# Optimization experiments

Measured on AMD Instinct MI355X. Metric: run time of the kernel, lower is better.

Reference implementation:

```python
import jax, jax.numpy as jnp
import numpy as np
from jax import lax

T = 512
DELTA_T = 2.0 ** -10
MAX_RATE = 200.0
DECAY1, DECAY2, CONST, THRESH = 0.25, 0.25, 0.5, 0.3
B = 32


def _conv(x, w):
    # VALID 5x5 conv, stride 1, NCHW / OIHW
    return lax.conv_general_dilated(x, w, (1, 1), 'VALID',
                                    dimension_numbers=('NCHW', 'OIHW', 'NCHW'))


def _avgpool2(x):
    b, c, h, w = x.shape
    return x.reshape(b, c, h // 2, 2, w // 2, 2).mean(axis=(3, 5))


def _lif(drive, mem1, mem2, spike):
    # two-compartment LIF membrane update with soft reset via (1 - spike)
    mem1 = mem1 * DECAY1 * (1.0 - spike) + drive
    mem2 = mem2 * DECAY2 * (1.0 - spike) + CONST * mem1
    new_spike = (mem2 > THRESH).astype(drive.dtype)
    return mem1, mem2, new_spike


def setup_inputs() -> dict:
    key = jax.random.key(0)
    ks = jax.random.split(key, 6)
    image = jax.random.uniform(ks[0], (B, 1, 32, 32), dtype=jnp.float32)
    def kaiming(k, shape, fan_in):
        return jax.random.normal(k, shape, dtype=jnp.float32) / np.float32(np.sqrt(fan_in))
    w1 = kaiming(ks[1], (6, 1, 5, 5), 1 * 25)
    w2 = kaiming(ks[2], (16, 6, 5, 5), 6 * 25)
    w3 = kaiming(ks[3], (120, 16, 5, 5), 16 * 25)
    fw1 = kaiming(ks[4], (84, 120), 120)
    fw2 = kaiming(ks[5], (10, 84), 84)
    return {'image': image, 'w1': w1, 'w2': w2, 'w3': w3, 'fw1': fw1, 'fw2': fw2}


def reference(image, w1, w2, w3, fw1, fw2):
    dt = image.dtype
    z = lambda *s: (jnp.zeros(s, dt), jnp.zeros(s, dt), jnp.zeros(s, dt))
    state0 = (z(B, 6, 28, 28), z(B, 6, 14, 14), z(B, 16, 10, 10),
              z(B, 16, 5, 5), z(B, 120, 1, 1), z(B, 84), z(B, 10),
              jnp.zeros((B, 10), dt))
    keys = jax.random.split(jax.random.key(1), T)

    def step(state, k):
        s1, s2, s3, s4, s5, s6, s7, acc = state
        x = (image * MAX_RATE * DELTA_T > jax.random.uniform(k, image.shape, dtype=dt)).astype(dt)
        s1 = _lif(_conv(x, w1), *s1)
        s2 = _lif(_avgpool2(s1[2]), *s2)
        s3 = _lif(_conv(s2[2], w2), *s3)
        s4 = _lif(_avgpool2(s3[2]), *s4)
        s5 = _lif(_conv(s4[2], w3), *s5)
        s6 = _lif(s5[2].reshape(B, -1) @ fw1.T, *s6)
        s7 = _lif(s6[2] @ fw2.T, *s7)
        acc = acc + s7[2]
        return (s1, s2, s3, s4, s5, s6, s7, acc), None

    final, _ = lax.scan(step, state0, keys)
    return final[-1] / T
```

## Files before the change

### kernel.cpp

```cpp
#include <hip/hip_runtime.h>
#include <cstdint>

#define TSTEPS 512

typedef __attribute__((ext_vector_type(2))) float f32x2;

__device__ __forceinline__ void tfr(uint32_t& x0, uint32_t& x1, int r) {
    x0 += x1;
    x1 = (x1 << r) | (x1 >> (32 - r));
    x1 ^= x0;
}

__device__ __forceinline__ void threefry2x32(uint32_t k0, uint32_t k1,
                                             uint32_t c0, uint32_t c1,
                                             uint32_t& o0, uint32_t& o1) {
    uint32_t k2 = k0 ^ k1 ^ 0x1BD11BDAu;
    uint32_t x0 = c0 + k0, x1 = c1 + k1;
    tfr(x0, x1, 13); tfr(x0, x1, 15); tfr(x0, x1, 26); tfr(x0, x1, 6);
    x0 += k1; x1 += k2 + 1u;
    tfr(x0, x1, 17); tfr(x0, x1, 29); tfr(x0, x1, 16); tfr(x0, x1, 24);
    x0 += k2; x1 += k0 + 2u;
    tfr(x0, x1, 13); tfr(x0, x1, 15); tfr(x0, x1, 26); tfr(x0, x1, 6);
    x0 += k0; x1 += k1 + 3u;
    tfr(x0, x1, 17); tfr(x0, x1, 29); tfr(x0, x1, 16); tfr(x0, x1, 24);
    x0 += k1; x1 += k2 + 4u;
    tfr(x0, x1, 13); tfr(x0, x1, 15); tfr(x0, x1, 26); tfr(x0, x1, 6);
    o0 = x0 + k2; o1 = x1 + k0 + 5u;
}

__global__ void k_keys(uint2* __restrict__ keys) {
    int t = threadIdx.x;
    uint32_t o0, o1;
    threefry2x32(0u, 1u, 0u, (uint32_t)t, o0, o1);
    keys[t] = make_uint2(o0, o1);
}

__global__ __launch_bounds__(256) void k_encode(const float* __restrict__ img,
                                                const uint2* __restrict__ keys,
                                                uint32_t* __restrict__ sxm) {
    int gid = blockIdx.x * 256 + threadIdx.x;
    int t = gid >> 15;
    int n = gid & 32767;
    uint2 k = keys[t];
    uint32_t o0, o1;
    threefry2x32(k.x, k.y, 0u, (uint32_t)n, o0, o1);
    float u = __uint_as_float((o0 >> 9) | 0x3f800000u) - 1.0f;
    float p = (img[n] * 200.0f) * 0.0009765625f;
    unsigned long long bal = __ballot(p > u);
    if ((threadIdx.x & 63) == 0) {
        int word = n >> 5;
        sxm[t * 1024 + word]     = (uint32_t)bal;
        sxm[t * 1024 + word + 1] = (uint32_t)(bal >> 32);
    }
}

__device__ __forceinline__ void lif(float drive, float& m1, float& m2, float& sp) {
    float r = 1.0f - sp;
    m1 = m1 * 0.25f * r + drive;
    m2 = m2 * 0.25f * r + 0.5f * m1;
    sp = (m2 > 0.3f) ? 1.0f : 0.0f;
}

#define SMEM_DW 22606
#define SMEM_BYTES (SMEM_DW * 4)

__global__ __launch_bounds__(1024) void k_main(
        const float* __restrict__ w1g, const float* __restrict__ w2g,
        const float* __restrict__ w3g, const float* __restrict__ fw1g,
        const float* __restrict__ fw2g, const uint32_t* __restrict__ sxm,
        float* __restrict__ out) {
    extern __shared__ float smem[];
    const f32x2* tbl2v = (const f32x2*)smem;
    const f32x2* tbl1p = (const f32x2*)(smem + 15840);
    float*    fw2s  = smem + 16830;
    float*    s3f   = smem + 17670;
    float*    s4f   = smem + 20870;
    float*    s5f   = smem + 21670;
    float*    s6f   = smem + 21910;
    uint32_t* s1m   = (uint32_t*)(smem + 22078);
    uint32_t* s2m   = (uint32_t*)(smem + 22414);

    const int tid  = threadIdx.x;
    const int lane = tid & 63;
    const int b    = blockIdx.x;

    for (int e = tid; e < 990; e += 1024) {
        int pr = e / 330, r = e % 330;
        int ky = r / 66, r2 = r % 66;
        int m = r2 >> 1, half = r2 & 1;
        int c = pr * 2 + half;
        float v = 0.0f;
        #pragma unroll
        for (int kx = 0; kx < 5; ++kx)
            if ((m >> kx) & 1) v += w1g[c * 25 + ky * 5 + kx];
        smem[15840 + e] = v;
    }
    for (int e = tid; e < 7680; e += 1024) {
        int cg = e / 960, r = e % 960, ci = r / 160, r2 = r % 160;
        int ky = r2 >> 5, m = r2 & 31;
        float v0 = 0.0f, v1 = 0.0f;
        #pragma unroll
        for (int kx = 0; kx < 5; ++kx)
            if ((m >> kx) & 1) {
                v0 += w2g[((cg * 2) * 6 + ci) * 25 + ky * 5 + kx];
                v1 += w2g[((cg * 2 + 1) * 6 + ci) * 25 + ky * 5 + kx];
            }
        smem[2 * (((cg * 6 + ci) * 5 + ky) * 33 + m)]     = v0;
        smem[2 * (((cg * 6 + ci) * 5 + ky) * 33 + m) + 1] = v1;
    }
    for (int e = tid; e < 840; e += 1024) fw2s[e] = fw2g[e];
    for (int e = tid; e < 4936; e += 1024) smem[17670 + e] = 0.0f;

    float fw1r[15];
    if (tid < 672) {
        int o = tid >> 3, j = tid & 7;
        #pragma unroll
        for (int i = 0; i < 15; ++i) fw1r[i] = fw1g[o * 120 + j * 15 + i];
    }

    float m1a[6] = {}, m2a[6] = {}, spa[6] = {};
    float m1b0 = 0, m2b0 = 0, spb0 = 0, m1b1 = 0, m2b1 = 0, spb1 = 0;
    float m1c0 = 0, m2c0 = 0, spc0 = 0, m1c1 = 0, m2c1 = 0, spc1 = 0;
    float m1d = 0, m2d = 0, spd = 0;
    float m1e = 0, m2e = 0, spe = 0;
    float m1f = 0, m2f = 0, spf = 0;
    float m1g = 0, m2g = 0, spg = 0, accf = 0.0f;

    uint32_t sx_cur = 0u, sx_nxt = 0u;
    if (tid < 896) {
        int half = lane >> 5, row = lane & 31;
        sx_cur = sxm[half * 1024 + b * 32 + row];
        sx_nxt = sxm[(half + 2) * 1024 + b * 32 + row];
    }

    __syncthreads();

    #pragma unroll 1
    for (int tau = 0; tau < TSTEPS / 2 + 6; ++tau) {
        const int p = tau & 1, q = p ^ 1;

        if (tid < 896) {
            const int y = tid >> 5, x = tid & 31;
            const bool valid = (x < 28);
            #pragma unroll
            for (int u = 0; u < 2; ++u) {
                uint32_t* s1w = s1m + p * 336 + u * 168;
                f32x2 d01 = {0.0f, 0.0f}, d23 = {0.0f, 0.0f}, d45 = {0.0f, 0.0f};
                #pragma unroll
                for (int ky = 0; ky < 5; ++ky) {
                    uint32_t row = (uint32_t)__shfl((int)sx_cur, u * 32 + y + ky, 64);
                    uint32_t mm = (row >> x) & 31u;
                    d01 += tbl1p[(0 * 5 + ky) * 33 + mm];
                    d23 += tbl1p[(1 * 5 + ky) * 33 + mm];
                    d45 += tbl1p[(2 * 5 + ky) * 33 + mm];
                }
                lif(d01[0], m1a[0], m2a[0], spa[0]);
                lif(d01[1], m1a[1], m2a[1], spa[1]);
                lif(d23[0], m1a[2], m2a[2], spa[2]);
                lif(d23[1], m1a[3], m2a[3], spa[3]);
                lif(d45[0], m1a[4], m2a[4], spa[4]);
                lif(d45[1], m1a[5], m2a[5], spa[5]);
                #pragma unroll
                for (int c = 0; c < 6; ++c) {
                    unsigned long long bal = __ballot(valid && (spa[c] > 0.0f));
                    if (lane == 0)       s1w[c * 28 + (tid >> 6) * 2]     = (uint32_t)bal;
                    else if (lane == 32) s1w[c * 28 + (tid >> 6) * 2 + 1] = (uint32_t)(bal >> 32);
                }
            }
            sx_cur = sx_nxt;
            int tt = 2 * tau + 4 + (lane >> 5);
            if (tt > TSTEPS - 1) tt = TSTEPS - 1;
            sx_nxt = sxm[tt * 1024 + b * 32 + (lane & 31)];
        }

        #pragma unroll
        for (int u = 0; u < 2; ++u) {
            const uint32_t* s1r = s1m + q * 336 + u * 168;
            uint32_t*       s2w = s2m + p * 192 + u * 96;
            {
                const int c = tid / 224, rem = tid % 224;
                const int yy = rem >> 4, xx = rem & 15;
                const bool valid = (xx < 14);
                uint32_t r0 = s1r[c * 28 + 2 * yy];
                uint32_t r1 = s1r[c * 28 + 2 * yy + 1];
                uint32_t sh = 2u * (uint32_t)xx;
                int cnt = (int)((r0 >> sh) & 1u) + (int)((r0 >> (sh + 1)) & 1u)
                        + (int)((r1 >> sh) & 1u) + (int)((r1 >> (sh + 1)) & 1u);
                lif(0.25f * (float)cnt, m1b0, m2b0, spb0);
                unsigned long long bal = __ballot(valid && (spb0 > 0.0f));
                if ((lane & 15) == 0)
                    s2w[tid >> 4] = (uint32_t)((bal >> (lane & 48)) & 0x3FFFull);
            }
            if (tid >= 704) {
                const int slot = tid + 320;
                const int c = slot / 224, rem = slot % 224;
                const int yy = rem >> 4, xx = rem & 15;
                const bool valid = (xx < 14);
                uint32_t r0 = s1r[c * 28 + 2 * yy];
                uint32_t r1 = s1r[c * 28 + 2 * yy + 1];
                uint32_t sh = 2u * (uint32_t)xx;
                int cnt = (int)((r0 >> sh) & 1u) + (int)((r0 >> (sh + 1)) & 1u)
                        + (int)((r1 >> sh) & 1u) + (int)((r1 >> (sh + 1)) & 1u);
                lif(0.25f * (float)cnt, m1b1, m2b1, spb1);
                unsigned long long bal = __ballot(valid && (spb1 > 0.0f));
                if ((lane & 15) == 0)
                    s2w[slot >> 4] = (uint32_t)((bal >> (lane & 48)) & 0x3FFFull);
            }
        }

        if (tid >= 224) {
            const int uu = tid - 224;
            const int px = uu >> 3, cg = uu & 7;
            const int yy = px / 10, xx = px % 10;
            #pragma unroll
            for (int u = 0; u < 2; ++u) {
                const uint32_t* s2r = s2m + q * 192 + u * 96;
                float*          s3w = s3f + p * 3200 + u * 1600;
                f32x2 d01 = {0.0f, 0.0f};
                #pragma unroll
                for (int ci = 0; ci < 6; ++ci) {
                    #pragma unroll
                    for (int ky = 0; ky < 5; ++ky) {
                        uint32_t mm = (s2r[ci * 14 + yy + ky] >> xx) & 31u;
                        d01 += tbl2v[((cg * 6 + ci) * 5 + ky) * 33 + mm];
                    }
                }
                lif(d01[0], m1c0, m2c0, spc0);
                lif(d01[1], m1c1, m2c1, spc1);
                s3w[(cg * 2) * 100 + px]     = spc0;
                s3w[(cg * 2 + 1) * 100 + px] = spc1;
            }
        }

        if (tid < 400) {
            const int c = tid / 25, rem = tid % 25;
            const int yy = rem / 5, xx = rem % 5;
            #pragma unroll
            for (int u = 0; u < 2; ++u) {
                const float* pp = s3f + q * 3200 + u * 1600 + c * 100 + yy * 20 + xx * 2;
                float sum = pp[0] + pp[1] + pp[10] + pp[11];
                lif(0.25f * sum, m1d, m2d, spd);
                (s4f + p * 800 + u * 400)[tid] = spd;
            }
        }

        if (tid < 960) {
            const int cc = tid >> 3, j = tid & 7;
            const float2* wp  = (const float2*)(w3g + cc * 400 + j * 50);
            const float2* sp0 = (const float2*)(s4f + q * 800 + 0 * 400 + j * 50);
            const float2* sp1 = (const float2*)(s4f + q * 800 + 1 * 400 + j * 50);
            float sum0 = 0.0f, sum1 = 0.0f;
            #pragma unroll
            for (int i = 0; i < 25; ++i) {
                float2 w = wp[i];
                float2 a = sp0[i];
                float2 c2 = sp1[i];
                sum0 = fmaf(w.y, a.y,  fmaf(w.x, a.x,  sum0));
                sum1 = fmaf(w.y, c2.y, fmaf(w.x, c2.x, sum1));
            }
            sum0 += __shfl_xor(sum0, 1, 64);
            sum0 += __shfl_xor(sum0, 2, 64);
            sum0 += __shfl_xor(sum0, 4, 64);
            sum1 += __shfl_xor(sum1, 1, 64);
            sum1 += __shfl_xor(sum1, 2, 64);
            sum1 += __shfl_xor(sum1, 4, 64);
            if (j == 0) {
                lif(sum0, m1e, m2e, spe); (s5f + p * 240 + 0 * 120)[cc] = spe;
                lif(sum1, m1e, m2e, spe); (s5f + p * 240 + 1 * 120)[cc] = spe;
            }
        }

        if (tid < 672) {
            const int j = tid & 7;
            #pragma unroll
            for (int u = 0; u < 2; ++u) {
                const float* s5r = s5f + q * 240 + u * 120;
                float sum = 0.0f;
                #pragma unroll
                for (int i = 0; i < 15; ++i) sum = fmaf(fw1r[i], s5r[j * 15 + i], sum);
                sum += __shfl_xor(sum, 1, 64);
                sum += __shfl_xor(sum, 2, 64);
                sum += __shfl_xor(sum, 4, 64);
                if (j == 0) { lif(sum, m1f, m2f, spf); (s6f + p * 168 + u * 84)[tid >> 3] = spf; }
            }
        }

        if (tid < 40) {
            const int o = tid >> 2, j = tid & 3;
            #pragma unroll
            for (int u = 0; u < 2; ++u) {
                const float* s6r = s6f + q * 168 + u * 84;
                float sum = 0.0f;
                #pragma unroll
                for (int i = 0; i < 21; ++i)
                    sum = fmaf(fw2s[o * 84 + j * 21 + i], s6r[j * 21 + i], sum);
                sum += __shfl_xor(sum, 1, 64);
                sum += __shfl_xor(sum, 2, 64);
                if (j == 0) { lif(sum, m1g, m2g, spg); accf += spg; }
            }
        }

        __syncthreads();
    }

    if (tid < 40 && (tid & 3) == 0)
        out[b * 10 + (tid >> 2)] = accf * (1.0f / 512.0f);
}

extern "C" void kernel_launch(void* const* d_in, const int* in_sizes, int n_in,
                              void* d_out, int out_size, void* d_ws, size_t ws_size,
                              hipStream_t stream) {
    const float* img = (const float*)d_in[0];
    const float* w1  = (const float*)d_in[1];
    const float* w2  = (const float*)d_in[2];
    const float* w3  = (const float*)d_in[3];
    const float* fw1 = (const float*)d_in[4];
    const float* fw2 = (const float*)d_in[5];
    float* out = (float*)d_out;

    uint2*    keys = (uint2*)d_ws;
    uint32_t* sxm  = (uint32_t*)((char*)d_ws + 4096);

    k_keys<<<1, 512, 0, stream>>>(keys);
    k_encode<<<(TSTEPS * 32768) / 256, 256, 0, stream>>>(img, keys, sxm);

    (void)hipFuncSetAttribute(reinterpret_cast<const void*>(k_main),
                              hipFuncAttributeMaxDynamicSharedMemorySize,
                              SMEM_BYTES);
    k_main<<<32, 1024, SMEM_BYTES, stream>>>(w1, w2, w3, fw1, fw2, sxm, out);
}
```

Baseline: 2.093 ms.

## Rotate per-wave stage order to stagger pipeline stages across waves

Wraps the seven per-timestep layer stages in a loop with a switch keyed on (wave id + k) mod 7, so each wavefront runs the stages in a different rotated order. The goal is to spread out contention for the same LDS tables, global weights and ALU work, so waves are not all hitting the same resource at once. The conv1 table goes back to a plain scalar float layout and conv2 now uses float2 loads with scalar accumulation. The change adds a runtime switch and loop overhead, and it may hurt instruction-cache behaviour and register allocation because the stage code can no longer be straight-lined.

```diff
diff --git a/kernel.cpp b/kernel.cpp
--- a/kernel.cpp
+++ b/kernel.cpp
@@ -2,8 +2,6 @@
 #include <cstdint>
 
 #define TSTEPS 512
-
-typedef __attribute__((ext_vector_type(2))) float f32x2;
 
 __device__ __forceinline__ void tfr(uint32_t& x0, uint32_t& x1, int r) {
     x0 += x1;
@@ -70,8 +68,8 @@
         const float* __restrict__ fw2g, const uint32_t* __restrict__ sxm,
         float* __restrict__ out) {
     extern __shared__ float smem[];
-    const f32x2* tbl2v = (const f32x2*)smem;
-    const f32x2* tbl1p = (const f32x2*)(smem + 15840);
+    float2*   tbl2v = (float2*)smem;
+    float*    tbl1  = smem + 15840;
     float*    fw2s  = smem + 16830;
     float*    s3f   = smem + 17670;
     float*    s4f   = smem + 20870;
@@ -82,18 +80,16 @@
 
     const int tid  = threadIdx.x;
     const int lane = tid & 63;
+    const int wid  = tid >> 6;
     const int b    = blockIdx.x;
 
-    for (int e = tid; e < 990; e += 1024) {
-        int pr = e / 330, r = e % 330;
-        int ky = r / 66, r2 = r % 66;
-        int m = r2 >> 1, half = r2 & 1;
-        int c = pr * 2 + half;
+    for (int e = tid; e < 960; e += 1024) {
+        int c = e / 160, r = e % 160, ky = r >> 5, m = r & 31;
         float v = 0.0f;
         #pragma unroll
         for (int kx = 0; kx < 5; ++kx)
             if ((m >> kx) & 1) v += w1g[c * 25 + ky * 5 + kx];
-        smem[15840 + e] = v;
+        tbl1[(c * 5 + ky) * 33 + m] = v;
     }
     for (int e = tid; e < 7680; e += 1024) {
         int cg = e / 960, r = e % 960, ci = r / 160, r2 = r % 160;
@@ -105,8 +101,7 @@
                 v0 += w2g[((cg * 2) * 6 + ci) * 25 + ky * 5 + kx];
                 v1 += w2g[((cg * 2 + 1) * 6 + ci) * 25 + ky * 5 + kx];
             }
-        smem[2 * (((cg * 6 + ci) * 5 + ky) * 33 + m)]     = v0;
-        smem[2 * (((cg * 6 + ci) * 5 + ky) * 33 + m) + 1] = v1;
+        tbl2v[((cg * 6 + ci) * 5 + ky) * 33 + m] = make_float2(v0, v1);
     }
     for (int e = tid; e < 840; e += 1024) fw2s[e] = fw2g[e];
     for (int e = tid; e < 4936; e += 1024) smem[17670 + e] = 0.0f;
@@ -139,164 +134,181 @@
     for (int tau = 0; tau < TSTEPS / 2 + 6; ++tau) {
         const int p = tau & 1, q = p ^ 1;
 
-        if (tid < 896) {
-            const int y = tid >> 5, x = tid & 31;
-            const bool valid = (x < 28);
+        #pragma unroll 1
+        for (int k = 0; k < 7; ++k) {
+            switch ((wid + k) % 7) {
+            case 0:
+            if (tid < 896) {
+                const int y = tid >> 5, x = tid & 31;
+                const bool valid = (x < 28);
+                #pragma unroll
+                for (int u = 0; u < 2; ++u) {
+                    uint32_t* s1w = s1m + p * 336 + u * 168;
+                    float d[6];
+                    #pragma unroll
+                    for (int c = 0; c < 6; ++c) d[c] = 0.0f;
+                    #pragma unroll
+                    for (int ky = 0; ky < 5; ++ky) {
+                        uint32_t row = (uint32_t)__shfl((int)sx_cur, u * 32 + y + ky, 64);
+                        uint32_t mm = (row >> x) & 31u;
+                        #pragma unroll
+                        for (int c = 0; c < 6; ++c) d[c] += tbl1[(c * 5 + ky) * 33 + mm];
+                    }
+                    #pragma unroll
+                    for (int c = 0; c < 6; ++c) lif(d[c], m1a[c], m2a[c], spa[c]);
+                    #pragma unroll
+                    for (int c = 0; c < 6; ++c) {
+                        unsigned long long bal = __ballot(valid && (spa[c] > 0.0f));
+                        if (lane == 0)       s1w[c * 28 + (tid >> 6) * 2]     = (uint32_t)bal;
+                        else if (lane == 32) s1w[c * 28 + (tid >> 6) * 2 + 1] = (uint32_t)(bal >> 32);
+                    }
+                }
+                sx_cur = sx_nxt;
+                int tt = 2 * tau + 4 + (lane >> 5);
+                if (tt > TSTEPS - 1) tt = TSTEPS - 1;
+                sx_nxt = sxm[tt * 1024 + b * 32 + (lane & 31)];
+            }
+            break;
+
+            case 1:
             #pragma unroll
             for (int u = 0; u < 2; ++u) {
-                uint32_t* s1w = s1m + p * 336 + u * 168;
-                f32x2 d01 = {0.0f, 0.0f}, d23 = {0.0f, 0.0f}, d45 = {0.0f, 0.0f};
-                #pragma unroll
-                for (int ky = 0; ky < 5; ++ky) {
-                    uint32_t row = (uint32_t)__shfl((int)sx_cur, u * 32 + y + ky, 64);
-                    uint32_t mm = (row >> x) & 31u;
-                    d01 += tbl1p[(0 * 5 + ky) * 33 + mm];
-                    d23 += tbl1p[(1 * 5 + ky) * 33 + mm];
-                    d45 += tbl1p[(2 * 5 + ky) * 33 + mm];
-                }
-                lif(d01[0], m1a[0], m2a[0], spa[0]);
-                lif(d01[1], m1a[1], m2a[1], spa[1]);
-                lif(d23[0], m1a[2], m2a[2], spa[2]);
-                lif(d23[1], m1a[3], m2a[3], spa[3]);
-                lif(d45[0], m1a[4], m2a[4], spa[4]);
-                lif(d45[1], m1a[5], m2a[5], spa[5]);
-                #pragma unroll
-                for (int c = 0; c < 6; ++c) {
-                    unsigned long long bal = __ballot(valid && (spa[c] > 0.0f));
-                    if (lane == 0)       s1w[c * 28 + (tid >> 6) * 2]     = (uint32_t)bal;
-                    else if (lane == 32) s1w[c * 28 + (tid >> 6) * 2 + 1] = (uint32_t)(bal >> 32);
-                }
-            }
-            sx_cur = sx_nxt;
-            int tt = 2 * tau + 4 + (lane >> 5);
-            if (tt > TSTEPS - 1) tt = TSTEPS - 1;
-            sx_nxt = sxm[tt * 1024 + b * 32 + (lane & 31)];
-        }
-
-        #pragma unroll
-        for (int u = 0; u < 2; ++u) {
-            const uint32_t* s1r = s1m + q * 336 + u * 168;
-            uint32_t*       s2w = s2m + p * 192 + u * 96;
-            {
-                const int c = tid / 224, rem = tid % 224;
-                const int yy = rem >> 4, xx = rem & 15;
-                const bool valid = (xx < 14);
-                uint32_t r0 = s1r[c * 28 + 2 * yy];
-                uint32_t r1 = s1r[c * 28 + 2 * yy + 1];
-                uint32_t sh = 2u * (uint32_t)xx;
-                int cnt = (int)((r0 >> sh) & 1u) + (int)((r0 >> (sh + 1)) & 1u)
-                        + (int)((r1 >> sh) & 1u) + (int)((r1 >> (sh + 1)) & 1u);
-                lif(0.25f * (float)cnt, m1b0, m2b0, spb0);
-                unsigned long long bal = __ballot(valid && (spb0 > 0.0f));
-                if ((lane & 15) == 0)
-                    s2w[tid >> 4] = (uint32_t)((bal >> (lane & 48)) & 0x3FFFull);
-            }
-            if (tid >= 704) {
-                const int slot = tid + 320;
-                const int c = slot / 224, rem = slot % 224;
-                const int yy = rem >> 4, xx = rem & 15;
-                const bool valid = (xx < 14);
-                uint32_t r0 = s1r[c * 28 + 2 * yy];
-                uint32_t r1 = s1r[c * 28 + 2 * yy + 1];
-                uint32_t sh = 2u * (uint32_t)xx;
-                int cnt = (int)((r0 >> sh) & 1u) + (int)((r0 >> (sh + 1)) & 1u)
-                        + (int)((r1 >> sh) & 1u) + (int)((r1 >> (sh + 1)) & 1u);
-                lif(0.25f * (float)cnt, m1b1, m2b1, spb1);
-                unsigned long long bal = __ballot(valid && (spb1 > 0.0f));
-                if ((lane & 15) == 0)
-                    s2w[slot >> 4] = (uint32_t)((bal >> (lane & 48)) & 0x3FFFull);
-            }
-        }
-
-        if (tid >= 224) {
-            const int uu = tid - 224;
-            const int px = uu >> 3, cg = uu & 7;
-            const int yy = px / 10, xx = px % 10;
-            #pragma unroll
-            for (int u = 0; u < 2; ++u) {
-                const uint32_t* s2r = s2m + q * 192 + u * 96;
-                float*          s3w = s3f + p * 3200 + u * 1600;
-                f32x2 d01 = {0.0f, 0.0f};
-                #pragma unroll
-                for (int ci = 0; ci < 6; ++ci) {
-                    #pragma unroll
-                    for (int ky = 0; ky < 5; ++ky) {
-                        uint32_t mm = (s2r[ci * 14 + yy + ky] >> xx) & 31u;
-                        d01 += tbl2v[((cg * 6 + ci) * 5 + ky) * 33 + mm];
+                const uint32_t* s1r = s1m + q * 336 + u * 168;
+                uint32_t*       s2w = s2m + p * 192 + u * 96;
+                {
+                    const int c = tid / 224, rem = tid % 224;
+                    const int yy = rem >> 4, xx = rem & 15;
+                    const bool valid = (xx < 14);
+                    uint32_t r0 = s1r[c * 28 + 2 * yy];
+                    uint32_t r1 = s1r[c * 28 + 2 * yy + 1];
+                    uint32_t sh = 2u * (uint32_t)xx;
+                    int cnt = (int)((r0 >> sh) & 1u) + (int)((r0 >> (sh + 1)) & 1u)
+                            + (int)((r1 >> sh) & 1u) + (int)((r1 >> (sh + 1)) & 1u);
+                    lif(0.25f * (float)cnt, m1b0, m2b0, spb0);
+                    unsigned long long bal = __ballot(valid && (spb0 > 0.0f));
+                    if ((lane & 15) == 0)
+                        s2w[tid >> 4] = (uint32_t)((bal >> (lane & 48)) & 0x3FFFull);
+                }
+                if (tid >= 704) {
+                    const int slot = tid + 320;
+                    const int c = slot / 224, rem = slot % 224;
+                    const int yy = rem >> 4, xx = rem & 15;
+                    const bool valid = (xx < 14);
+                    uint32_t r0 = s1r[c * 28 + 2 * yy];
+                    uint32_t r1 = s1r[c * 28 + 2 * yy + 1];
+                    uint32_t sh = 2u * (uint32_t)xx;
+                    int cnt = (int)((r0 >> sh) & 1u) + (int)((r0 >> (sh + 1)) & 1u)
+                            + (int)((r1 >> sh) & 1u) + (int)((r1 >> (sh + 1)) & 1u);
+                    lif(0.25f * (float)cnt, m1b1, m2b1, spb1);
+                    unsigned long long bal = __ballot(valid && (spb1 > 0.0f));
+                    if ((lane & 15) == 0)
+                        s2w[slot >> 4] = (uint32_t)((bal >> (lane & 48)) & 0x3FFFull);
+                }
+            }
+            break;
+
+            case 2:
+            if (tid >= 224) {
+                const int uu = tid - 224;
+                const int px = uu >> 3, cg = uu & 7;
+                const int yy = px / 10, xx = px % 10;
+                #pragma unroll
+                for (int u = 0; u < 2; ++u) {
+                    const uint32_t* s2r = s2m + q * 192 + u * 96;
+                    float*          s3w = s3f + p * 3200 + u * 1600;
+                    float d0 = 0.0f, d1 = 0.0f;
+                    #pragma unroll
+                    for (int ci = 0; ci < 6; ++ci) {
+                        #pragma unroll
+                        for (int ky = 0; ky < 5; ++ky) {
+                            uint32_t mm = (s2r[ci * 14 + yy + ky] >> xx) & 31u;
+                            float2 v = tbl2v[((cg * 6 + ci) * 5 + ky) * 33 + mm];
+                            d0 += v.x; d1 += v.y;
+                        }
                     }
-                }
-                lif(d01[0], m1c0, m2c0, spc0);
-                lif(d01[1], m1c1, m2c1, spc1);
-                s3w[(cg * 2) * 100 + px]     = spc0;
-                s3w[(cg * 2 + 1) * 100 + px] = spc1;
-            }
-        }
-
-        if (tid < 400) {
-            const int c = tid / 25, rem = tid % 25;
-            const int yy = rem / 5, xx = rem % 5;
-            #pragma unroll
-            for (int u = 0; u < 2; ++u) {
-                const float* pp = s3f + q * 3200 + u * 1600 + c * 100 + yy * 20 + xx * 2;
-                float sum = pp[0] + pp[1] + pp[10] + pp[11];
-                lif(0.25f * sum, m1d, m2d, spd);
-                (s4f + p * 800 + u * 400)[tid] = spd;
-            }
-        }
-
-        if (tid < 960) {
-            const int cc = tid >> 3, j = tid & 7;
-            const float2* wp  = (const float2*)(w3g + cc * 400 + j * 50);
-            const float2* sp0 = (const float2*)(s4f + q * 800 + 0 * 400 + j * 50);
-            const float2* sp1 = (const float2*)(s4f + q * 800 + 1 * 400 + j * 50);
-            float sum0 = 0.0f, sum1 = 0.0f;
-            #pragma unroll
-            for (int i = 0; i < 25; ++i) {
-                float2 w = wp[i];
-                float2 a = sp0[i];
-                float2 c2 = sp1[i];
-                sum0 = fmaf(w.y, a.y,  fmaf(w.x, a.x,  sum0));
-                sum1 = fmaf(w.y, c2.y, fmaf(w.x, c2.x, sum1));
-            }
-            sum0 += __shfl_xor(sum0, 1, 64);
-            sum0 += __shfl_xor(sum0, 2, 64);
-            sum0 += __shfl_xor(sum0, 4, 64);
-            sum1 += __shfl_xor(sum1, 1, 64);
-            sum1 += __shfl_xor(sum1, 2, 64);
-            sum1 += __shfl_xor(sum1, 4, 64);
-            if (j == 0) {
-                lif(sum0, m1e, m2e, spe); (s5f + p * 240 + 0 * 120)[cc] = spe;
-                lif(sum1, m1e, m2e, spe); (s5f + p * 240 + 1 * 120)[cc] = spe;
-            }
-        }
-
-        if (tid < 672) {
-            const int j = tid & 7;
-            #pragma unroll
-            for (int u = 0; u < 2; ++u) {
-                const float* s5r = s5f + q * 240 + u * 120;
-                float sum = 0.0f;
-                #pragma unroll
-                for (int i = 0; i < 15; ++i) sum = fmaf(fw1r[i], s5r[j * 15 + i], sum);
-                sum += __shfl_xor(sum, 1, 64);
-                sum += __shfl_xor(sum, 2, 64);
-                sum += __shfl_xor(sum, 4, 64);
-                if (j == 0) { lif(sum, m1f, m2f, spf); (s6f + p * 168 + u * 84)[tid >> 3] = spf; }
-            }
-        }
-
-        if (tid < 40) {
-            const int o = tid >> 2, j = tid & 3;
-            #pragma unroll
-            for (int u = 0; u < 2; ++u) {
-                const float* s6r = s6f + q * 168 + u * 84;
-                float sum = 0.0f;
-                #pragma unroll
-                for (int i = 0; i < 21; ++i)
-                    sum = fmaf(fw2s[o * 84 + j * 21 + i], s6r[j * 21 + i], sum);
-                sum += __shfl_xor(sum, 1, 64);
-                sum += __shfl_xor(sum, 2, 64);
-                if (j == 0) { lif(sum, m1g, m2g, spg); accf += spg; }
+                    lif(d0, m1c0, m2c0, spc0);
+                    lif(d1, m1c1, m2c1, spc1);
+                    s3w[(cg * 2) * 100 + px]     = spc0;
+                    s3w[(cg * 2 + 1) * 100 + px] = spc1;
+                }
+            }
+            break;
+
+            case 3:
+            if (tid < 400) {
+                const int c = tid / 25, rem = tid % 25;
+                const int yy = rem / 5, xx = rem % 5;
+                #pragma unroll
+                for (int u = 0; u < 2; ++u) {
+                    const float* pp = s3f + q * 3200 + u * 1600 + c * 100 + yy * 20 + xx * 2;
+                    float sum = pp[0] + pp[1] + pp[10] + pp[11];
+                    lif(0.25f * sum, m1d, m2d, spd);
+                    (s4f + p * 800 + u * 400)[tid] = spd;
+                }
+            }
+            break;
+
+            case 4:
+            if (tid < 960) {
+                const int cc = tid >> 3, j = tid & 7;
+                const float2* wp  = (const float2*)(w3g + cc * 400 + j * 50);
+                const float2* sp0 = (const float2*)(s4f + q * 800 + 0 * 400 + j * 50);
+                const float2* sp1 = (const float2*)(s4f + q * 800 + 1 * 400 + j * 50);
+                float sum0 = 0.0f, sum1 = 0.0f;
+                #pragma unroll
+                for (int i = 0; i < 25; ++i) {
+                    float2 w = wp[i];
+                    float2 a = sp0[i];
+                    float2 c2 = sp1[i];
+                    sum0 = fmaf(w.y, a.y,  fmaf(w.x, a.x,  sum0));
+                    sum1 = fmaf(w.y, c2.y, fmaf(w.x, c2.x, sum1));
+                }
+                sum0 += __shfl_xor(sum0, 1, 64);
+                sum0 += __shfl_xor(sum0, 2, 64);
+                sum0 += __shfl_xor(sum0, 4, 64);
+                sum1 += __shfl_xor(sum1, 1, 64);
+                sum1 += __shfl_xor(sum1, 2, 64);
+                sum1 += __shfl_xor(sum1, 4, 64);
+                if (j == 0) {
+                    lif(sum0, m1e, m2e, spe); (s5f + p * 240 + 0 * 120)[cc] = spe;
+                    lif(sum1, m1e, m2e, spe); (s5f + p * 240 + 1 * 120)[cc] = spe;
+                }
+            }
+            break;
+
+            case 5:
+            if (tid < 672) {
+                const int j = tid & 7;
+                #pragma unroll
+                for (int u = 0; u < 2; ++u) {
+                    const float* s5r = s5f + q * 240 + u * 120;
+                    float sum = 0.0f;
+                    #pragma unroll
+                    for (int i = 0; i < 15; ++i) sum = fmaf(fw1r[i], s5r[j * 15 + i], sum);
+                    sum += __shfl_xor(sum, 1, 64);
+                    sum += __shfl_xor(sum, 2, 64);
+                    sum += __shfl_xor(sum, 4, 64);
+                    if (j == 0) { lif(sum, m1f, m2f, spf); (s6f + p * 168 + u * 84)[tid >> 3] = spf; }
+                }
+            }
+            break;
+
+            default:
+            if (tid < 40) {
+                const int o = tid >> 2, j = tid & 3;
+                #pragma unroll
+                for (int u = 0; u < 2; ++u) {
+                    const float* s6r = s6f + q * 168 + u * 84;
+                    float sum = 0.0f;
+                    #pragma unroll
+                    for (int i = 0; i < 21; ++i)
+                        sum = fmaf(fw2s[o * 84 + j * 21 + i], s6r[j * 21 + i], sum);
+                    sum += __shfl_xor(sum, 1, 64);
+                    sum += __shfl_xor(sum, 2, 64);
+                    if (j == 0) { lif(sum, m1g, m2g, spg); accf += spg; }
+                }
+            }
+            break;
             }
         }
 
```

Result: slower. 2.462 ms (+17.6%).
